# Performance work log

Hardware: AMD Instinct MI355X
Metric: run time of the kernel (lower is better)

## Reference

```python
import jax, jax.numpy as jnp
import numpy as np

B, N, K, H, Cin, Cout = 2, 8192, 16, 4, 64, 128
D = Cout // H  # head_dim = 32


def setup_inputs() -> dict:
    key = jax.random.key(0)
    ks = jax.random.split(key, 16)
    x = jax.random.normal(ks[0], (B, N, Cin), jnp.float32)
    pos = jax.random.uniform(ks[1], (B, N, 3), jnp.float32)
    # KNN indices (torch.no_grad in original): pairwise squared distance + top_k
    sq = jnp.sum(pos * pos, -1)
    d2 = sq[:, :, None] - 2.0 * jnp.einsum('bnc,bmc->bnm', pos, pos) + sq[:, None, :]
    _, idx = jax.lax.top_k(-d2, K)  # (B, N, K) int32

    def lin(k, fin, fout):
        kw, kb = jax.random.split(k)
        lim = 1.0 / np.sqrt(fin)
        W = jax.random.uniform(kw, (fin, fout), jnp.float32, -lim, lim)
        b = jax.random.uniform(kb, (fout,), jnp.float32, -lim, lim)
        return W, b

    Wq, bq = lin(ks[2], Cin, Cout)
    Wkv, bkv = lin(ks[3], Cin, 2 * Cout)
    Wp1, bp1 = lin(ks[4], 3, Cout)
    Wp2, bp2 = lin(ks[5], Cout, Cout)
    Wa1, ba1 = lin(ks[6], Cout, Cout)
    Wa2, ba2 = lin(ks[7], Cout, Cout)
    Wo, bo = lin(ks[8], Cout, Cout)
    return dict(x=x, pos=pos, idx=idx, Wq=Wq, bq=bq, Wkv=Wkv, bkv=bkv,
                Wp1=Wp1, bp1=bp1, Wp2=Wp2, bp2=bp2,
                Wa1=Wa1, ba1=ba1, Wa2=Wa2, ba2=ba2, Wo=Wo, bo=bo)


def reference(x, pos, idx, Wq, bq, Wkv, bkv, Wp1, bp1, Wp2, bp2,
              Wa1, ba1, Wa2, ba2, Wo, bo):
    q = (x @ Wq + bq).reshape(B, N, H, D)
    kv = x @ Wkv + bkv
    k, v = kv[..., :Cout].reshape(B, N, H, D), kv[..., Cout:].reshape(B, N, H, D)
    bix = jnp.arange(B)[:, None, None]
    pos_n = pos[bix, idx]          # (B,N,K,3)
    k_n = k[bix, idx]              # (B,N,K,H,D)
    v_n = v[bix, idx]              # (B,N,K,H,D)
    pos_diff = pos[:, :, None, :] - pos_n
    pos_enc = jax.nn.relu(pos_diff @ Wp1 + bp1) @ Wp2 + bp2   # (B,N,K,Cout)
    pos_enc_h = pos_enc.reshape(B, N, K, H, D)
    rel = (k_n - q[:, :, None] + pos_enc_h).reshape(B, N, K, Cout)
    attn = jax.nn.relu(rel @ Wa1 + ba1) @ Wa2 + ba2           # (B,N,K,Cout)
    attn = jax.nn.softmax(attn.reshape(B, N, K, H, D), axis=2)
    agg = jnp.sum(attn * (v_n + pos_enc_h), axis=2).reshape(B, N, Cout)
    return agg @ Wo + bo
```

## Files before the change

kernel.cpp:

```cpp
#include <hip/hip_runtime.h>
#include <stdint.h>


typedef __attribute__((ext_vector_type(8))) short short8;
typedef __attribute__((ext_vector_type(4))) float f32x4;
typedef __attribute__((ext_vector_type(4))) unsigned int u32x4;

#define NN_TOT 16384
#define PES 136

__device__ __forceinline__ uint32_t pk_bf16(float a, float b) {
  uint32_t r;
  asm("v_cvt_pk_bf16_f32 %0, %1, %2" : "=v"(r) : "v"(a), "v"(b));
  return r;
}
__device__ __forceinline__ float lo_f(uint32_t p) {
  return __builtin_bit_cast(float, p << 16);
}
__device__ __forceinline__ float hi_f(uint32_t p) {
  return __builtin_bit_cast(float, p & 0xffff0000u);
}
__device__ __forceinline__ short f2bf_rne(float f) {
  uint32_t u = __builtin_bit_cast(uint32_t, f);
  uint32_t r = (u + 0x7FFFu + ((u >> 16) & 1u)) >> 16;
  return (short)r;
}
__device__ __forceinline__ float bf2f(unsigned short s) {
  uint32_t u = ((uint32_t)s) << 16;
  return __builtin_bit_cast(float, u);
}

__global__ __launch_bounds__(256) void prep_frags(
    const float* __restrict__ Wq, const float* __restrict__ Wkv,
    const float* __restrict__ Wp2, const float* __restrict__ Wa1,
    const float* __restrict__ Wa2, const float* __restrict__ Wo,
    short* __restrict__ fqh, short* __restrict__ fql,
    short* __restrict__ fwp2, short* __restrict__ fwa1, short* __restrict__ fwa2,
    short* __restrict__ fwoh, short* __restrict__ fwol) {
  int r = blockIdx.x * 256 + threadIdx.x;
  if (r < 3072) {
    int t = r >> 7, rem = r & 127, s = rem >> 6, lane = rem & 63;
    int quad = lane >> 4, l15 = lane & 15;
    int col = t * 16 + l15;
    #pragma unroll
    for (int j = 0; j < 8; j++) {
      int i = 32 * s + quad * 8 + j;
      float wv = (col < 128) ? Wq[i * 128 + col] : Wkv[i * 256 + (col - 128)];
      short hi = f2bf_rne(wv);
      fqh[r * 8 + j] = hi;
      fql[r * 8 + j] = f2bf_rne(wv - bf2f((unsigned short)hi));
    }
  } else {
    int r2 = r - 3072;
    int mat = r2 >> 11;
    int rr = r2 & 2047;
    int t = rr >> 8, rem = rr & 255, s = rem >> 6, lane = rem & 63;
    int quad = lane >> 4, l15 = lane & 15;
    int col = t * 16 + l15;
    const float* W = (mat == 0) ? Wp2 : (mat == 1) ? Wa1 : (mat == 2) ? Wa2 : Wo;
    #pragma unroll
    for (int j = 0; j < 8; j++) {
      int i = 32 * s + quad * 8 + j;
      float wv = W[i * 128 + col];
      short hi = f2bf_rne(wv);
      if (mat == 3) {
        fwoh[rr * 8 + j] = hi;
        fwol[rr * 8 + j] = f2bf_rne(wv - bf2f((unsigned short)hi));
      } else if (mat == 0) fwp2[rr * 8 + j] = hi;
      else if (mat == 1)   fwa1[rr * 8 + j] = hi;
      else                 fwa2[rr * 8 + j] = hi;
    }
  }
}

__device__ __forceinline__ void split_frag(const f32x4 x0, const f32x4 x1,
                                           short8& ah, short8& al) {
  uint32_t h01 = pk_bf16(x0[0], x0[1]);
  uint32_t h23 = pk_bf16(x0[2], x0[3]);
  uint32_t h45 = pk_bf16(x1[0], x1[1]);
  uint32_t h67 = pk_bf16(x1[2], x1[3]);
  u32x4 hh = {h01, h23, h45, h67};
  ah = __builtin_bit_cast(short8, hh);
  uint32_t l01 = pk_bf16(x0[0] - lo_f(h01), x0[1] - hi_f(h01));
  uint32_t l23 = pk_bf16(x0[2] - lo_f(h23), x0[3] - hi_f(h23));
  uint32_t l45 = pk_bf16(x1[0] - lo_f(h45), x1[1] - hi_f(h45));
  uint32_t l67 = pk_bf16(x1[2] - lo_f(h67), x1[3] - hi_f(h67));
  u32x4 ll = {l01, l23, l45, l67};
  al = __builtin_bit_cast(short8, ll);
}

__global__ __launch_bounds__(256) void qkv_kernel(
    const float* __restrict__ x, const float* __restrict__ bq,
    const float* __restrict__ bkv,
    const short* __restrict__ fqh, const short* __restrict__ fql,
    float* __restrict__ q, float* __restrict__ k, float* __restrict__ v) {
  int wid = blockIdx.x * 4 + (threadIdx.x >> 6);
  int g = wid / 6, r6 = wid % 6, sec = r6 >> 1, hf = r6 & 1;
  int lane = threadIdx.x & 63, quad = lane >> 4, l15 = lane & 15;
  int base = g * 16;

  short8 ah[2], al[2];
  #pragma unroll
  for (int s = 0; s < 2; s++) {
    const float* xp = x + (base + l15) * 64 + 32 * s + quad * 8;
    split_frag(*reinterpret_cast<const f32x4*>(xp),
               *reinterpret_cast<const f32x4*>(xp + 4), ah[s], al[s]);
  }

  #pragma unroll
  for (int tt = 0; tt < 4; tt++) {
    int t = sec * 8 + hf * 4 + tt;
    f32x4 acc = {0.f, 0.f, 0.f, 0.f};
    #pragma unroll
    for (int s = 0; s < 2; s++) {
      short8 bh = *reinterpret_cast<const short8*>(fqh + ((t * 2 + s) * 64 + lane) * 8);
      short8 bl = *reinterpret_cast<const short8*>(fql + ((t * 2 + s) * 64 + lane) * 8);
      acc = __builtin_amdgcn_mfma_f32_16x16x32_bf16(ah[s], bh, acc, 0, 0, 0);
      acc = __builtin_amdgcn_mfma_f32_16x16x32_bf16(ah[s], bl, acc, 0, 0, 0);
      acc = __builtin_amdgcn_mfma_f32_16x16x32_bf16(al[s], bh, acc, 0, 0, 0);
    }
    int cc = t * 16 + l15;
    float biasv;
    float* dst;
    if (cc < 128)      { biasv = bq[cc];        dst = q + cc; }
    else if (cc < 256) { biasv = bkv[cc - 128]; dst = k + (cc - 128); }
    else               { biasv = bkv[cc - 128]; dst = v + (cc - 256); }
    #pragma unroll
    for (int r = 0; r < 4; r++)
      dst[(base + quad * 4 + r) * 128] = acc[r] + biasv;
  }
}

__global__ __launch_bounds__(512, 2) void fused_attn_wo(
    const float* __restrict__ pos, const int* __restrict__ idx,
    const float* __restrict__ Wp1, const float* __restrict__ bp1,
    const float* __restrict__ bp2, const float* __restrict__ ba1,
    const float* __restrict__ ba2,
    const short* __restrict__ fw_all,
    const short* __restrict__ fwoh, const short* __restrict__ fwol,
    const float* __restrict__ bo,
    const float* __restrict__ qg, const float* __restrict__ kg,
    const float* __restrict__ vg, float* __restrict__ out) {
  __shared__ __align__(16) short sB[49152];
  __shared__ __align__(16) unsigned short stg[8][16 * PES];
  __shared__ __align__(16) float sagg[16][132];
  __shared__ float spd[8][2][16][3];
  __shared__ int sidx[8][2][16];

  const int tid = threadIdx.x;
  const int w = tid >> 6;
  const int lane = tid & 63;
  const int quad = lane >> 4, l15 = lane & 15;
  const int nb0 = blockIdx.x * 16;
  const int nbw = nb0 + w * 2;

  if (lane < 32) {
    int nn2 = lane >> 4, m = lane & 15;
    int node = nbw + nn2;
    int ji = idx[node * 16 + m];
    int jn = ((node >> 13) << 13) + ji;
    sidx[w][nn2][m] = jn;
    spd[w][nn2][m][0] = pos[node * 3 + 0] - pos[jn * 3 + 0];
    spd[w][nn2][m][1] = pos[node * 3 + 1] - pos[jn * 3 + 1];
    spd[w][nn2][m][2] = pos[node * 3 + 2] - pos[jn * 3 + 2];
  }

  {
    const u32x4* src = reinterpret_cast<const u32x4*>(fw_all);
    u32x4* dst = reinterpret_cast<u32x4*>(sB);
    #pragma unroll
    for (int i = 0; i < 12; i++) dst[tid + i * 512] = src[tid + i * 512];
  }
  __syncthreads();

  f32x4 kq0[2][4], kq1[2][4];
  #pragma unroll
  for (int nn2 = 0; nn2 < 2; nn2++) {
    const float* kp = kg + sidx[w][nn2][l15] * 128;
    const float* qp = qg + (nbw + nn2) * 128;
    #pragma unroll
    for (int s = 0; s < 4; s++) {
      int ch = 32 * s + quad * 8;
      f32x4 ka = *reinterpret_cast<const f32x4*>(kp + ch);
      f32x4 kb = *reinterpret_cast<const f32x4*>(kp + ch + 4);
      f32x4 qa = *reinterpret_cast<const f32x4*>(qp + ch);
      f32x4 qb = *reinterpret_cast<const f32x4*>(qp + ch + 4);
      kq0[nn2][s] = ka - qa;
      kq1[nn2][s] = kb - qb;
    }
  }

  short8 aP[2][4];
  {
    const int c0 = lane, c1 = lane + 64;
    float wp00 = Wp1[c0], wp01 = Wp1[128 + c0], wp02 = Wp1[256 + c0], bb0 = bp1[c0];
    float wp10 = Wp1[c1], wp11 = Wp1[128 + c1], wp12 = Wp1[256 + c1], bb1 = bp1[c1];
    #pragma unroll
    for (int nn2 = 0; nn2 < 2; nn2++) {
      #pragma unroll
      for (int m = 0; m < 16; m++) {
        float d0 = spd[w][nn2][m][0], d1 = spd[w][nn2][m][1], d2 = spd[w][nn2][m][2];
        float h0 = fmaxf(bb0 + d0 * wp00 + d1 * wp01 + d2 * wp02, 0.f);
        float h1 = fmaxf(bb1 + d0 * wp10 + d1 * wp11 + d2 * wp12, 0.f);
        uint32_t pck = pk_bf16(h0, h1);
        stg[w][m * PES + c0] = (unsigned short)pck;
        stg[w][m * PES + c1] = (unsigned short)(pck >> 16);
      }
      #pragma unroll
      for (int s = 0; s < 4; s++)
        aP[nn2][s] = *reinterpret_cast<const short8*>(&stg[w][l15 * PES + 32 * s + quad * 8]);
    }
  }

  f32x4 acc0[8], acc1[8];

  #pragma unroll
  for (int t = 0; t < 8; t++) { acc0[t] = (f32x4){0,0,0,0}; acc1[t] = (f32x4){0,0,0,0}; }
  #pragma unroll
  for (int s = 0; s < 4; s++) {
    #pragma unroll
    for (int t = 0; t < 8; t++) {
      short8 bf = *reinterpret_cast<const short8*>(sB + ((t * 4 + s) * 64 + lane) * 8);
      acc0[t] = __builtin_amdgcn_mfma_f32_16x16x32_bf16(aP[0][s], bf, acc0[t], 0, 0, 0);
      acc1[t] = __builtin_amdgcn_mfma_f32_16x16x32_bf16(aP[1][s], bf, acc1[t], 0, 0, 0);
    }
  }

  uint32_t pe_pk[2][8][2];
  short8 aR[2][4];
  #pragma unroll
  for (int nn2 = 0; nn2 < 2; nn2++) {
    f32x4* ac = nn2 ? acc1 : acc0;
    #pragma unroll
    for (int t = 0; t < 8; t++) {
      int c = 16 * t + l15;
      float bb = bp2[c];
      uint32_t p01 = pk_bf16(ac[t][0] + bb, ac[t][1] + bb);
      uint32_t p23 = pk_bf16(ac[t][2] + bb, ac[t][3] + bb);
      pe_pk[nn2][t][0] = p01;
      pe_pk[nn2][t][1] = p23;
      stg[w][(quad * 4 + 0) * PES + c] = (unsigned short)p01;
      stg[w][(quad * 4 + 1) * PES + c] = (unsigned short)(p01 >> 16);
      stg[w][(quad * 4 + 2) * PES + c] = (unsigned short)p23;
      stg[w][(quad * 4 + 3) * PES + c] = (unsigned short)(p23 >> 16);
    }
    #pragma unroll
    for (int s = 0; s < 4; s++)
      aR[nn2][s] = *reinterpret_cast<const short8*>(&stg[w][l15 * PES + 32 * s + quad * 8]);
  }

  short8 a2[2][4];
  #pragma unroll
  for (int nn2 = 0; nn2 < 2; nn2++) {
    #pragma unroll
    for (int s = 0; s < 4; s++) {
      short8 pp = aR[nn2][s];
      u32x4 av = {pk_bf16(kq0[nn2][s][0] + bf2f((unsigned short)pp[0]),
                          kq0[nn2][s][1] + bf2f((unsigned short)pp[1])),
                  pk_bf16(kq0[nn2][s][2] + bf2f((unsigned short)pp[2]),
                          kq0[nn2][s][3] + bf2f((unsigned short)pp[3])),
                  pk_bf16(kq1[nn2][s][0] + bf2f((unsigned short)pp[4]),
                          kq1[nn2][s][1] + bf2f((unsigned short)pp[5])),
                  pk_bf16(kq1[nn2][s][2] + bf2f((unsigned short)pp[6]),
                          kq1[nn2][s][3] + bf2f((unsigned short)pp[7]))};
      a2[nn2][s] = __builtin_bit_cast(short8, av);
    }
  }

  #pragma unroll
  for (int t = 0; t < 8; t++) { acc0[t] = (f32x4){0,0,0,0}; acc1[t] = (f32x4){0,0,0,0}; }
  #pragma unroll
  for (int s = 0; s < 4; s++) {
    #pragma unroll
    for (int t = 0; t < 8; t++) {
      short8 bf = *reinterpret_cast<const short8*>(sB + 16384 + ((t * 4 + s) * 64 + lane) * 8);
      acc0[t] = __builtin_amdgcn_mfma_f32_16x16x32_bf16(a2[0][s], bf, acc0[t], 0, 0, 0);
      acc1[t] = __builtin_amdgcn_mfma_f32_16x16x32_bf16(a2[1][s], bf, acc1[t], 0, 0, 0);
    }
  }

  short8 a3[2][4];
  #pragma unroll
  for (int nn2 = 0; nn2 < 2; nn2++) {
    f32x4* ac = nn2 ? acc1 : acc0;
    #pragma unroll
    for (int t = 0; t < 8; t++) {
      int c = 16 * t + l15;
      float bb = ba1[c];
      uint32_t p01 = pk_bf16(fmaxf(ac[t][0] + bb, 0.f), fmaxf(ac[t][1] + bb, 0.f));
      uint32_t p23 = pk_bf16(fmaxf(ac[t][2] + bb, 0.f), fmaxf(ac[t][3] + bb, 0.f));
      stg[w][(quad * 4 + 0) * PES + c] = (unsigned short)p01;
      stg[w][(quad * 4 + 1) * PES + c] = (unsigned short)(p01 >> 16);
      stg[w][(quad * 4 + 2) * PES + c] = (unsigned short)p23;
      stg[w][(quad * 4 + 3) * PES + c] = (unsigned short)(p23 >> 16);
    }
    #pragma unroll
    for (int s = 0; s < 4; s++)
      a3[nn2][s] = *reinterpret_cast<const short8*>(&stg[w][l15 * PES + 32 * s + quad * 8]);
  }

  #pragma unroll
  for (int t = 0; t < 8; t++) { acc0[t] = (f32x4){0,0,0,0}; acc1[t] = (f32x4){0,0,0,0}; }
  #pragma unroll
  for (int s = 0; s < 4; s++) {
    #pragma unroll
    for (int t = 0; t < 8; t++) {
      short8 bf = *reinterpret_cast<const short8*>(sB + 32768 + ((t * 4 + s) * 64 + lane) * 8);
      acc0[t] = __builtin_amdgcn_mfma_f32_16x16x32_bf16(a3[0][s], bf, acc0[t], 0, 0, 0);
      acc1[t] = __builtin_amdgcn_mfma_f32_16x16x32_bf16(a3[1][s], bf, acc1[t], 0, 0, 0);
    }
  }

  int vb[2][4];
  #pragma unroll
  for (int nn2 = 0; nn2 < 2; nn2++)
    #pragma unroll
    for (int r = 0; r < 4; r++)
      vb[nn2][r] = sidx[w][nn2][quad * 4 + r] * 128;

  #pragma unroll
  for (int t = 0; t < 8; t++) {
    int c = 16 * t + l15;
    float bb = ba2[c];
    #pragma unroll
    for (int nn2 = 0; nn2 < 2; nn2++) {
      f32x4* ac = nn2 ? acc1 : acc0;
      float g0 = ac[t][0] + bb, g1 = ac[t][1] + bb;
      float g2 = ac[t][2] + bb, g3 = ac[t][3] + bb;
      float mx = fmaxf(fmaxf(g0, g1), fmaxf(g2, g3));
      mx = fmaxf(mx, __shfl_xor(mx, 16));
      mx = fmaxf(mx, __shfl_xor(mx, 32));
      float e0 = __expf(g0 - mx), e1 = __expf(g1 - mx);
      float e2 = __expf(g2 - mx), e3 = __expf(g3 - mx);
      float ls = e0 + e1 + e2 + e3;
      ls += __shfl_xor(ls, 16);
      ls += __shfl_xor(ls, 32);
      float pe0 = lo_f(pe_pk[nn2][t][0]), pe1 = hi_f(pe_pk[nn2][t][0]);
      float pe2 = lo_f(pe_pk[nn2][t][1]), pe3 = hi_f(pe_pk[nn2][t][1]);
      float p = e0 * (vg[vb[nn2][0] + c] + pe0)
              + e1 * (vg[vb[nn2][1] + c] + pe1)
              + e2 * (vg[vb[nn2][2] + c] + pe2)
              + e3 * (vg[vb[nn2][3] + c] + pe3);
      p += __shfl_xor(p, 16);
      p += __shfl_xor(p, 32);
      if (quad == 0) sagg[w * 2 + nn2][c] = p * __builtin_amdgcn_rcpf(ls);
    }
  }
  __syncthreads();

  {
    short8 ah[4], al[4];
    #pragma unroll
    for (int s = 0; s < 4; s++) {
      f32x4 x0 = *reinterpret_cast<const f32x4*>(&sagg[l15][32 * s + quad * 8]);
      f32x4 x1 = *reinterpret_cast<const f32x4*>(&sagg[l15][32 * s + quad * 8 + 4]);
      split_frag(x0, x1, ah[s], al[s]);
    }
    f32x4 aw = {0.f, 0.f, 0.f, 0.f};
    #pragma unroll
    for (int s = 0; s < 4; s++) {
      short8 bh = *reinterpret_cast<const short8*>(fwoh + ((w * 4 + s) * 64 + lane) * 8);
      short8 bl = *reinterpret_cast<const short8*>(fwol + ((w * 4 + s) * 64 + lane) * 8);
      aw = __builtin_amdgcn_mfma_f32_16x16x32_bf16(ah[s], bh, aw, 0, 0, 0);
      aw = __builtin_amdgcn_mfma_f32_16x16x32_bf16(ah[s], bl, aw, 0, 0, 0);
      aw = __builtin_amdgcn_mfma_f32_16x16x32_bf16(al[s], bh, aw, 0, 0, 0);
    }
    int c = 16 * w + l15;
    float bb = bo[c];
    #pragma unroll
    for (int r = 0; r < 4; r++)
      out[(nb0 + quad * 4 + r) * 128 + c] = aw[r] + bb;
  }
}

extern "C" void kernel_launch(void* const* d_in, const int* in_sizes, int n_in,
                              void* d_out, int out_size, void* d_ws, size_t ws_size,
                              hipStream_t stream) {
  const float* x   = (const float*)d_in[0];
  const float* pos = (const float*)d_in[1];
  const int*   idx = (const int*)d_in[2];
  const float* Wq  = (const float*)d_in[3];
  const float* bq  = (const float*)d_in[4];
  const float* Wkv = (const float*)d_in[5];
  const float* bkv = (const float*)d_in[6];
  const float* Wp1 = (const float*)d_in[7];
  const float* bp1 = (const float*)d_in[8];
  const float* Wp2 = (const float*)d_in[9];
  const float* bp2 = (const float*)d_in[10];
  const float* Wa1 = (const float*)d_in[11];
  const float* ba1 = (const float*)d_in[12];
  const float* Wa2 = (const float*)d_in[13];
  const float* ba2 = (const float*)d_in[14];
  const float* Wo  = (const float*)d_in[15];
  const float* bo  = (const float*)d_in[16];

  char* ws = (char*)d_ws;
  short* fqh  = (short*)(ws + 0);
  short* fql  = (short*)(ws + 49152);
  short* fwp2 = (short*)(ws + 98304);
  short* fwa1 = (short*)(ws + 131072);
  short* fwa2 = (short*)(ws + 163840);
  short* fwoh = (short*)(ws + 196608);
  short* fwol = (short*)(ws + 229376);
  float* qb = (float*)(ws + 262144);
  float* kb = qb + NN_TOT * 128;
  float* vb = kb + NN_TOT * 128;

  prep_frags<<<44, 256, 0, stream>>>(Wq, Wkv, Wp2, Wa1, Wa2, Wo,
                                     fqh, fql, fwp2, fwa1, fwa2, fwoh, fwol);
  qkv_kernel<<<1536, 256, 0, stream>>>(x, bq, bkv, fqh, fql, qb, kb, vb);
  fused_attn_wo<<<1024, 512, 0, stream>>>(pos, idx, Wp1, bp1, bp2, ba1, ba2,
                                          fwp2, fwoh, fwol, bo,
                                          qb, kb, vb, (float*)d_out);
}
```

Baseline: 194.3 us.

## Store K/V as bf16, shrink shared weight buffer, stage QKV weights in LDS

The QKV projection kernel now has each block load its weight section into shared memory once and writes K and V as bf16 instead of fp32, which halves the traffic for the later random neighbor gathers. The attention kernel reuses one 32 KB shared buffer for the Wp2, Wa1 and Wa2 fragments in turn, reloading it between stages behind extra barriers, and aliases the aggregation buffer onto the staging area. The smaller shared footprint lets launch bounds target 4 blocks per SM instead of 2. In exchange it adds block-wide syncs and reloads on the critical path, and rounding K/V to bf16 costs some accuracy.

```diff
diff --git a/kernel.cpp b/kernel.cpp
--- a/kernel.cpp
+++ b/kernel.cpp
@@ -93,12 +93,28 @@
     const float* __restrict__ x, const float* __restrict__ bq,
     const float* __restrict__ bkv,
     const short* __restrict__ fqh, const short* __restrict__ fql,
-    float* __restrict__ q, float* __restrict__ k, float* __restrict__ v) {
-  int wid = blockIdx.x * 4 + (threadIdx.x >> 6);
-  int g = wid / 6, r6 = wid % 6, sec = r6 >> 1, hf = r6 & 1;
-  int lane = threadIdx.x & 63, quad = lane >> 4, l15 = lane & 15;
-  int base = g * 16;
-
+    float* __restrict__ q, unsigned short* __restrict__ ko,
+    unsigned short* __restrict__ vo) {
+  __shared__ __align__(16) short sBq[16384];
+  const int tid = threadIdx.x;
+  const int sec = blockIdx.x >> 8;
+  const int gq = blockIdx.x & 255;
+  const int w = tid >> 6, lane = tid & 63;
+  const int quad = lane >> 4, l15 = lane & 15;
+
+  {
+    const u32x4* sh = reinterpret_cast<const u32x4*>(fqh + sec * 8192);
+    const u32x4* sl = reinterpret_cast<const u32x4*>(fql + sec * 8192);
+    u32x4* dh = reinterpret_cast<u32x4*>(sBq);
+    u32x4* dl = reinterpret_cast<u32x4*>(sBq + 8192);
+    #pragma unroll
+    for (int i = 0; i < 4; i++) {
+      dh[tid + i * 256] = sh[tid + i * 256];
+      dl[tid + i * 256] = sl[tid + i * 256];
+    }
+  }
+
+  const int base = (gq * 4 + w) * 16;
   short8 ah[2], al[2];
   #pragma unroll
   for (int s = 0; s < 2; s++) {
@@ -106,46 +122,54 @@
     split_frag(*reinterpret_cast<const f32x4*>(xp),
                *reinterpret_cast<const f32x4*>(xp + 4), ah[s], al[s]);
   }
-
-  #pragma unroll
-  for (int tt = 0; tt < 4; tt++) {
-    int t = sec * 8 + hf * 4 + tt;
+  __syncthreads();
+
+  #pragma unroll
+  for (int tt = 0; tt < 8; tt++) {
     f32x4 acc = {0.f, 0.f, 0.f, 0.f};
     #pragma unroll
     for (int s = 0; s < 2; s++) {
-      short8 bh = *reinterpret_cast<const short8*>(fqh + ((t * 2 + s) * 64 + lane) * 8);
-      short8 bl = *reinterpret_cast<const short8*>(fql + ((t * 2 + s) * 64 + lane) * 8);
+      int rt = tt * 2 + s;
+      short8 bh = *reinterpret_cast<const short8*>(sBq + rt * 512 + lane * 8);
+      short8 bl = *reinterpret_cast<const short8*>(sBq + 8192 + rt * 512 + lane * 8);
       acc = __builtin_amdgcn_mfma_f32_16x16x32_bf16(ah[s], bh, acc, 0, 0, 0);
       acc = __builtin_amdgcn_mfma_f32_16x16x32_bf16(ah[s], bl, acc, 0, 0, 0);
       acc = __builtin_amdgcn_mfma_f32_16x16x32_bf16(al[s], bh, acc, 0, 0, 0);
     }
-    int cc = t * 16 + l15;
-    float biasv;
-    float* dst;
-    if (cc < 128)      { biasv = bq[cc];        dst = q + cc; }
-    else if (cc < 256) { biasv = bkv[cc - 128]; dst = k + (cc - 128); }
-    else               { biasv = bkv[cc - 128]; dst = v + (cc - 256); }
-    #pragma unroll
-    for (int r = 0; r < 4; r++)
-      dst[(base + quad * 4 + r) * 128] = acc[r] + biasv;
-  }
-}
-
-__global__ __launch_bounds__(512, 2) void fused_attn_wo(
+    int cl = tt * 16 + l15;
+    if (sec == 0) {
+      float bias = bq[cl];
+      #pragma unroll
+      for (int r = 0; r < 4; r++)
+        q[(base + quad * 4 + r) * 128 + cl] = acc[r] + bias;
+    } else {
+      float bias = bkv[(sec - 1) * 128 + cl];
+      unsigned short* dst = (sec == 1) ? ko : vo;
+      #pragma unroll
+      for (int r = 0; r < 4; r++) {
+        float vv = acc[r] + bias;
+        dst[(base + quad * 4 + r) * 128 + cl] = (unsigned short)pk_bf16(vv, vv);
+      }
+    }
+  }
+}
+
+__global__ __launch_bounds__(512, 4) void fused_attn_wo(
     const float* __restrict__ pos, const int* __restrict__ idx,
     const float* __restrict__ Wp1, const float* __restrict__ bp1,
     const float* __restrict__ bp2, const float* __restrict__ ba1,
     const float* __restrict__ ba2,
-    const short* __restrict__ fw_all,
+    const short* __restrict__ fwp2, const short* __restrict__ fwa1,
+    const short* __restrict__ fwa2,
     const short* __restrict__ fwoh, const short* __restrict__ fwol,
     const float* __restrict__ bo,
-    const float* __restrict__ qg, const float* __restrict__ kg,
-    const float* __restrict__ vg, float* __restrict__ out) {
-  __shared__ __align__(16) short sB[49152];
+    const float* __restrict__ qg, const unsigned short* __restrict__ kg,
+    const unsigned short* __restrict__ vg, float* __restrict__ out) {
+  __shared__ __align__(16) short sB[16384];
   __shared__ __align__(16) unsigned short stg[8][16 * PES];
-  __shared__ __align__(16) float sagg[16][132];
   __shared__ float spd[8][2][16][3];
   __shared__ int sidx[8][2][16];
+  float (*sagg)[132] = reinterpret_cast<float(*)[132]>(&stg[0][0]);
 
   const int tid = threadIdx.x;
   const int w = tid >> 6;
@@ -166,28 +190,10 @@
   }
 
   {
-    const u32x4* src = reinterpret_cast<const u32x4*>(fw_all);
-    u32x4* dst = reinterpret_cast<u32x4*>(sB);
-    #pragma unroll
-    for (int i = 0; i < 12; i++) dst[tid + i * 512] = src[tid + i * 512];
-  }
-  __syncthreads();
-
-  f32x4 kq0[2][4], kq1[2][4];
-  #pragma unroll
-  for (int nn2 = 0; nn2 < 2; nn2++) {
-    const float* kp = kg + sidx[w][nn2][l15] * 128;
-    const float* qp = qg + (nbw + nn2) * 128;
-    #pragma unroll
-    for (int s = 0; s < 4; s++) {
-      int ch = 32 * s + quad * 8;
-      f32x4 ka = *reinterpret_cast<const f32x4*>(kp + ch);
-      f32x4 kb = *reinterpret_cast<const f32x4*>(kp + ch + 4);
-      f32x4 qa = *reinterpret_cast<const f32x4*>(qp + ch);
-      f32x4 qb = *reinterpret_cast<const f32x4*>(qp + ch + 4);
-      kq0[nn2][s] = ka - qa;
-      kq1[nn2][s] = kb - qb;
-    }
+    const u32x4* s4 = reinterpret_cast<const u32x4*>(fwp2);
+    u32x4* d4 = reinterpret_cast<u32x4*>(sB);
+    #pragma unroll
+    for (int i = 0; i < 4; i++) d4[tid + i * 512] = s4[tid + i * 512];
   }
 
   short8 aP[2][4];
@@ -211,6 +217,16 @@
         aP[nn2][s] = *reinterpret_cast<const short8*>(&stg[w][l15 * PES + 32 * s + quad * 8]);
     }
   }
+  __syncthreads();
+
+  short8 k_pk[2][4];
+  #pragma unroll
+  for (int nn2 = 0; nn2 < 2; nn2++) {
+    const unsigned short* kp = kg + sidx[w][nn2][l15] * 128;
+    #pragma unroll
+    for (int s = 0; s < 4; s++)
+      k_pk[nn2][s] = *reinterpret_cast<const short8*>(kp + 32 * s + quad * 8);
+  }
 
   f32x4 acc0[8], acc1[8];
 
@@ -225,47 +241,53 @@
       acc1[t] = __builtin_amdgcn_mfma_f32_16x16x32_bf16(aP[1][s], bf, acc1[t], 0, 0, 0);
     }
   }
+  __syncthreads();
+
+  {
+    const u32x4* s4 = reinterpret_cast<const u32x4*>(fwa1);
+    u32x4* d4 = reinterpret_cast<u32x4*>(sB);
+    #pragma unroll
+    for (int i = 0; i < 4; i++) d4[tid + i * 512] = s4[tid + i * 512];
+  }
 
   uint32_t pe_pk[2][8][2];
-  short8 aR[2][4];
+  short8 a2[2][4];
   #pragma unroll
   for (int nn2 = 0; nn2 < 2; nn2++) {
     f32x4* ac = nn2 ? acc1 : acc0;
+    const float* qrow = qg + (nbw + nn2) * 128;
     #pragma unroll
     for (int t = 0; t < 8; t++) {
       int c = 16 * t + l15;
       float bb = bp2[c];
-      uint32_t p01 = pk_bf16(ac[t][0] + bb, ac[t][1] + bb);
-      uint32_t p23 = pk_bf16(ac[t][2] + bb, ac[t][3] + bb);
-      pe_pk[nn2][t][0] = p01;
-      pe_pk[nn2][t][1] = p23;
-      stg[w][(quad * 4 + 0) * PES + c] = (unsigned short)p01;
-      stg[w][(quad * 4 + 1) * PES + c] = (unsigned short)(p01 >> 16);
-      stg[w][(quad * 4 + 2) * PES + c] = (unsigned short)p23;
-      stg[w][(quad * 4 + 3) * PES + c] = (unsigned short)(p23 >> 16);
-    }
-    #pragma unroll
-    for (int s = 0; s < 4; s++)
-      aR[nn2][s] = *reinterpret_cast<const short8*>(&stg[w][l15 * PES + 32 * s + quad * 8]);
-  }
-
-  short8 a2[2][4];
-  #pragma unroll
-  for (int nn2 = 0; nn2 < 2; nn2++) {
+      float qv = qrow[c];
+      float f0 = ac[t][0] + bb, f1 = ac[t][1] + bb;
+      float f2 = ac[t][2] + bb, f3 = ac[t][3] + bb;
+      pe_pk[nn2][t][0] = pk_bf16(f0, f1);
+      pe_pk[nn2][t][1] = pk_bf16(f2, f3);
+      uint32_t g01 = pk_bf16(f0 - qv, f1 - qv);
+      uint32_t g23 = pk_bf16(f2 - qv, f3 - qv);
+      stg[w][(quad * 4 + 0) * PES + c] = (unsigned short)g01;
+      stg[w][(quad * 4 + 1) * PES + c] = (unsigned short)(g01 >> 16);
+      stg[w][(quad * 4 + 2) * PES + c] = (unsigned short)g23;
+      stg[w][(quad * 4 + 3) * PES + c] = (unsigned short)(g23 >> 16);
+    }
     #pragma unroll
     for (int s = 0; s < 4; s++) {
-      short8 pp = aR[nn2][s];
-      u32x4 av = {pk_bf16(kq0[nn2][s][0] + bf2f((unsigned short)pp[0]),
-                          kq0[nn2][s][1] + bf2f((unsigned short)pp[1])),
-                  pk_bf16(kq0[nn2][s][2] + bf2f((unsigned short)pp[2]),
-                          kq0[nn2][s][3] + bf2f((unsigned short)pp[3])),
-                  pk_bf16(kq1[nn2][s][0] + bf2f((unsigned short)pp[4]),
-                          kq1[nn2][s][1] + bf2f((unsigned short)pp[5])),
-                  pk_bf16(kq1[nn2][s][2] + bf2f((unsigned short)pp[6]),
-                          kq1[nn2][s][3] + bf2f((unsigned short)pp[7]))};
+      short8 pq = *reinterpret_cast<const short8*>(&stg[w][l15 * PES + 32 * s + quad * 8]);
+      short8 kk = k_pk[nn2][s];
+      u32x4 av = {pk_bf16(bf2f((unsigned short)kk[0]) + bf2f((unsigned short)pq[0]),
+                          bf2f((unsigned short)kk[1]) + bf2f((unsigned short)pq[1])),
+                  pk_bf16(bf2f((unsigned short)kk[2]) + bf2f((unsigned short)pq[2]),
+                          bf2f((unsigned short)kk[3]) + bf2f((unsigned short)pq[3])),
+                  pk_bf16(bf2f((unsigned short)kk[4]) + bf2f((unsigned short)pq[4]),
+                          bf2f((unsigned short)kk[5]) + bf2f((unsigned short)pq[5])),
+                  pk_bf16(bf2f((unsigned short)kk[6]) + bf2f((unsigned short)pq[6]),
+                          bf2f((unsigned short)kk[7]) + bf2f((unsigned short)pq[7]))};
       a2[nn2][s] = __builtin_bit_cast(short8, av);
     }
   }
+  __syncthreads();
 
   #pragma unroll
   for (int t = 0; t < 8; t++) { acc0[t] = (f32x4){0,0,0,0}; acc1[t] = (f32x4){0,0,0,0}; }
@@ -273,10 +295,18 @@
   for (int s = 0; s < 4; s++) {
     #pragma unroll
     for (int t = 0; t < 8; t++) {
-      short8 bf = *reinterpret_cast<const short8*>(sB + 16384 + ((t * 4 + s) * 64 + lane) * 8);
+      short8 bf = *reinterpret_cast<const short8*>(sB + ((t * 4 + s) * 64 + lane) * 8);
       acc0[t] = __builtin_amdgcn_mfma_f32_16x16x32_bf16(a2[0][s], bf, acc0[t], 0, 0, 0);
       acc1[t] = __builtin_amdgcn_mfma_f32_16x16x32_bf16(a2[1][s], bf, acc1[t], 0, 0, 0);
     }
+  }
+  __syncthreads();
+
+  {
+    const u32x4* s4 = reinterpret_cast<const u32x4*>(fwa2);
+    u32x4* d4 = reinterpret_cast<u32x4*>(sB);
+    #pragma unroll
+    for (int i = 0; i < 4; i++) d4[tid + i * 512] = s4[tid + i * 512];
   }
 
   short8 a3[2][4];
@@ -298,6 +328,7 @@
     for (int s = 0; s < 4; s++)
       a3[nn2][s] = *reinterpret_cast<const short8*>(&stg[w][l15 * PES + 32 * s + quad * 8]);
   }
+  __syncthreads();
 
   #pragma unroll
   for (int t = 0; t < 8; t++) { acc0[t] = (f32x4){0,0,0,0}; acc1[t] = (f32x4){0,0,0,0}; }
@@ -305,7 +336,7 @@
   for (int s = 0; s < 4; s++) {
     #pragma unroll
     for (int t = 0; t < 8; t++) {
-      short8 bf = *reinterpret_cast<const short8*>(sB + 32768 + ((t * 4 + s) * 64 + lane) * 8);
+      short8 bf = *reinterpret_cast<const short8*>(sB + ((t * 4 + s) * 64 + lane) * 8);
       acc0[t] = __builtin_amdgcn_mfma_f32_16x16x32_bf16(a3[0][s], bf, acc0[t], 0, 0, 0);
       acc1[t] = __builtin_amdgcn_mfma_f32_16x16x32_bf16(a3[1][s], bf, acc1[t], 0, 0, 0);
     }
@@ -337,10 +368,10 @@
       ls += __shfl_xor(ls, 32);
       float pe0 = lo_f(pe_pk[nn2][t][0]), pe1 = hi_f(pe_pk[nn2][t][0]);
       float pe2 = lo_f(pe_pk[nn2][t][1]), pe3 = hi_f(pe_pk[nn2][t][1]);
-      float p = e0 * (vg[vb[nn2][0] + c] + pe0)
-              + e1 * (vg[vb[nn2][1] + c] + pe1)
-              + e2 * (vg[vb[nn2][2] + c] + pe2)
-              + e3 * (vg[vb[nn2][3] + c] + pe3);
+      float p = e0 * (bf2f(vg[vb[nn2][0] + c]) + pe0)
+              + e1 * (bf2f(vg[vb[nn2][1] + c]) + pe1)
+              + e2 * (bf2f(vg[vb[nn2][2] + c]) + pe2)
+              + e3 * (bf2f(vg[vb[nn2][3] + c]) + pe3);
       p += __shfl_xor(p, 16);
       p += __shfl_xor(p, 32);
       if (quad == 0) sagg[w * 2 + nn2][c] = p * __builtin_amdgcn_rcpf(ls);
@@ -403,13 +434,13 @@
   short* fwoh = (short*)(ws + 196608);
   short* fwol = (short*)(ws + 229376);
   float* qb = (float*)(ws + 262144);
-  float* kb = qb + NN_TOT * 128;
-  float* vb = kb + NN_TOT * 128;
+  unsigned short* kb = (unsigned short*)(ws + 262144 + 8388608);
+  unsigned short* vb = kb + NN_TOT * 128;
 
   prep_frags<<<44, 256, 0, stream>>>(Wq, Wkv, Wp2, Wa1, Wa2, Wo,
                                      fqh, fql, fwp2, fwa1, fwa2, fwoh, fwol);
-  qkv_kernel<<<1536, 256, 0, stream>>>(x, bq, bkv, fqh, fql, qb, kb, vb);
+  qkv_kernel<<<768, 256, 0, stream>>>(x, bq, bkv, fqh, fql, qb, kb, vb);
   fused_attn_wo<<<1024, 512, 0, stream>>>(pos, idx, Wp1, bp1, bp2, ba1, ba2,
-                                          fwp2, fwoh, fwol, bo,
+                                          fwp2, fwa1, fwa2, fwoh, fwol, bo,
                                           qb, kb, vb, (float*)d_out);
 }
```

Result: faster. 187.1 us (-3.7%).
